# Kernel tuning notes

Measured on AMD Instinct MI355X. Metric: run time of the kernel, lower is better.

The kernel has to match this reference:

```python
import jax, jax.numpy as jnp
import numpy as np

COST_W = {'cls': 1.0, 'center': 0.0, 'obj_ness': 0.0, 'giou': 2.0}
IOU_THRES = 0.25
MAX_DYN = 10
EPS = 1e-6
N_PRED, N_GT, N_CLS = 65536, 128, 256


def _to_bbox(centers, sizes):
    # center/size -> (x1,y1,z1,x2,y2,z2)
    return jnp.concatenate([centers - sizes / 2.0, centers + sizes / 2.0], axis=-1)


def _giou_3d(b1, b2):
    # b1 [N,6], b2 [M,6] -> giou [N,M] (axis_aligned_bbox_overlaps_3d, mode='giou')
    vol1 = jnp.prod(b1[:, 3:] - b1[:, :3], axis=-1)  # [N]
    vol2 = jnp.prod(b2[:, 3:] - b2[:, :3], axis=-1)  # [M]
    lt = jnp.maximum(b1[:, None, :3], b2[None, :, :3])  # [N,M,3]
    rb = jnp.minimum(b1[:, None, 3:], b2[None, :, 3:])
    overlap = jnp.prod(jnp.clip(rb - lt, 0.0), axis=-1)  # [N,M]
    union = jnp.maximum(vol1[:, None] + vol2[None, :] - overlap, EPS)
    iou = overlap / union
    elt = jnp.minimum(b1[:, None, :3], b2[None, :, :3])
    erb = jnp.maximum(b1[:, None, 3:], b2[None, :, 3:])
    enclose = jnp.maximum(jnp.prod(jnp.clip(erb - elt, 0.0), axis=-1), EPS)
    return iou - (enclose - union) / enclose


def _lsa(cost):
    # Jonker-Volgenant shortest-augmenting-path LAP (same optimum as
    # scipy.optimize.linear_sum_assignment). cost [n, m], n <= m.
    # Returns col4row[n]: column matched to each row.
    n, m = cost.shape
    u = np.zeros(n, np.float64)
    v = np.zeros(m, np.float64)
    col4row = np.full(n, -1, np.int64)
    row4col = np.full(m, -1, np.int64)
    cost = cost.astype(np.float64)
    for cur in range(n):
        shortest = np.full(m, np.inf)
        path = np.full(m, -1, np.int64)
        SC = np.zeros(m, bool)
        SR = []
        i, min_val, sink = cur, 0.0, -1
        while sink == -1:
            SR.append(i)
            r = min_val + cost[i] - u[i] - v
            upd = (~SC) & (r < shortest)
            shortest = np.where(upd, r, shortest)
            path = np.where(upd, i, path)
            masked = np.where(SC, np.inf, shortest)
            j = int(masked.argmin())
            min_val = masked[j]
            SC[j] = True
            if row4col[j] == -1:
                sink = j
            else:
                i = int(row4col[j])
        u[cur] += min_val
        for i2 in SR:
            if i2 != cur:
                u[i2] += min_val - shortest[col4row[i2]]
        v[SC] -= min_val - shortest[SC]
        j = sink
        while True:
            i2 = int(path[j])
            row4col[j] = i2
            col4row[i2], j = j, col4row[i2]
            if i2 == cur:
                break
    return col4row


def _dynamic_assign(giou, used0, order):
    # Sequential greedy IoU-threshold assignment over gts (ascending max-iou).
    NEG = jnp.float32(-1e9)
    n_pred = giou.shape[0]

    def step(used, gt_idx):
        col = giou[:, gt_idx]
        vals = jnp.where((col > IOU_THRES) & (~used), col, NEG)
        topv, topi = jax.lax.top_k(vals, MAX_DYN)
        valid = topv > NEG
        used = used | jnp.zeros((n_pred,), bool).at[topi].set(valid)
        return used, (jnp.where(valid, topi, -1), jnp.where(valid, gt_idx, -1))

    _, (dp, dg) = jax.lax.scan(step, used0, order)
    return dp.reshape(-1), dg.reshape(-1)  # padded with -1 where invalid


def setup_inputs() -> dict:
    key = jax.random.key(0)
    k = jax.random.split(key, 7)
    return {
        'all_centers': jax.random.normal(k[0], (N_PRED, 3), jnp.float32),
        'all_sizes': jax.random.uniform(k[1], (N_PRED, 3), jnp.float32),
        'all_cls': jax.random.normal(k[2], (N_PRED, N_CLS), jnp.float32),
        'all_objness': jax.random.normal(k[3], (N_PRED,), jnp.float32),
        'gt_centers': jax.random.normal(k[4], (N_GT, 3), jnp.float32),
        'gt_sizes': jax.random.uniform(k[5], (N_GT, 3), jnp.float32),
        'gt_labels': jax.random.randint(k[6], (N_GT,), 0, N_CLS, jnp.int64),
    }


def reference(all_centers, all_sizes, all_cls, all_objness, gt_centers, gt_sizes, gt_labels):
    pred_bbox = _to_bbox(all_centers, all_sizes)
    gt_bbox = _to_bbox(gt_centers, gt_sizes)
    giou = _giou_3d(pred_bbox, gt_bbox)  # [N, M]
    cost_class = -jax.nn.sigmoid(all_cls)[:, gt_labels]  # [N, M]
    cost_center = jnp.sum(jnp.abs(all_centers[:, None, :] - gt_centers[None, :, :]), axis=-1)  # cdist p=1
    cost_obj = -jax.nn.sigmoid(all_objness)[:, None]  # [N, 1]
    total_cost = (COST_W['cls'] * cost_class + COST_W['center'] * cost_center
                  + COST_W['obj_ness'] * cost_obj + COST_W['giou'] * (-giou))
    # Hungarian on transposed cost (M <= N): same optimal pairing as scipy on [N, M].
    col4row = _lsa(np.asarray(jax.device_get(total_cost)).T)
    pred_indices = jnp.asarray(col4row, jnp.int64)       # matched pred per gt
    gt_indices = jnp.arange(gt_labels.shape[0], dtype=jnp.int64)
    used0 = jnp.zeros((giou.shape[0],), bool).at[pred_indices].set(True)
    order = jnp.argsort(jnp.max(giou, axis=0))
    dp, dg = _dynamic_assign(giou, used0, order)
    combined_preds = jnp.concatenate([pred_indices, dp.astype(jnp.int64)])
    combined_gts = jnp.concatenate([gt_indices, dg.astype(jnp.int64)])
    return combined_preds, combined_gts
```

## Files before the change

kernel.cpp:

```cpp
#include <hip/hip_runtime.h>
#include <hip/hip_bf16.h>
#include <math.h>

#define NPRED 65536
#define NGT   128
#define NCLS  256
#define CAP   12288
#define VCAP  160
#define VSLOT 129
#define NLIST 129
#define LSTRIDE 132
#define KEEP  2048
#define KMIN  1418
#define GSPLIT 4
#define GPB   (NGT / GSPLIT)
#define SENT_I 0x7FFFFFFF


__device__ __forceinline__ unsigned f2u(float f) {
    unsigned u = __float_as_uint(f);
    return (u & 0x80000000u) ? ~u : (u | 0x80000000u);
}
__device__ __forceinline__ float u2f(unsigned x) {
    unsigned u = (x & 0x80000000u) ? (x ^ 0x80000000u) : ~x;
    return __uint_as_float(u);
}
__device__ __forceinline__ unsigned long long d2u(double d) {
    unsigned long long u = (unsigned long long)__double_as_longlong(d);
    return (u & 0x8000000000000000ull) ? ~u : (u | 0x8000000000000000ull);
}
__device__ __forceinline__ double u2d(unsigned long long x) {
    unsigned long long u = (x & 0x8000000000000000ull) ? (x ^ 0x8000000000000000ull) : ~x;
    return __longlong_as_double((long long)u);
}

__device__ __forceinline__ float giou3d(
    float pl0, float pl1, float pl2, float ph0, float ph1, float ph2, float pvol,
    float gl0, float gl1, float gl2, float gh0, float gh1, float gh2, float gvol)
{
#pragma clang fp contract(off)
    float c0 = fmaxf(fminf(ph0, gh0) - fmaxf(pl0, gl0), 0.0f);
    float c1 = fmaxf(fminf(ph1, gh1) - fmaxf(pl1, gl1), 0.0f);
    float c2 = fmaxf(fminf(ph2, gh2) - fmaxf(pl2, gl2), 0.0f);
    float overlap = (c0 * c1) * c2;
    float uni = fmaxf((pvol + gvol) - overlap, 1e-6f);
    float iou = overlap / uni;
    float e0 = fmaxf(fmaxf(ph0, gh0) - fminf(pl0, gl0), 0.0f);
    float e1 = fmaxf(fmaxf(ph1, gh1) - fminf(pl1, gl1), 0.0f);
    float e2 = fmaxf(fmaxf(ph2, gh2) - fminf(pl2, gl2), 0.0f);
    float enc = fmaxf((e0 * e1) * e2, 1e-6f);
    return iou - (enc - uni) / enc;
}


__global__ __launch_bounds__(256) void k_gather(
    const float* __restrict__ cls, const int* __restrict__ lab,
    float* __restrict__ costT,
    int* __restrict__ ccnt, unsigned* __restrict__ cmax, int* __restrict__ failFlag)
{
#pragma clang fp contract(off)
    __shared__ float tile[64][NCLS + 1];
    __shared__ int labl[NGT];
    int tid = threadIdx.x;
    int p0 = blockIdx.x * 64;
    if (blockIdx.x == 0) {
        if (tid < NGT) { ccnt[tid] = 0; cmax[tid] = 0u; }
        if (tid == 0) *failFlag = 0;
    }
    if (tid < NGT) labl[tid] = lab[tid];
    for (int it = 0; it < 16; ++it) {
        int row = it * 4 + (tid >> 6);
        int col = (tid & 63) * 4;
        const float4 v = *(const float4*)&cls[(size_t)(p0 + row) * NCLS + col];
        tile[row][col + 0] = v.x; tile[row][col + 1] = v.y;
        tile[row][col + 2] = v.z; tile[row][col + 3] = v.w;
    }
    __syncthreads();
    int lane = tid & 63;
    for (int rep = 0; rep < 32; ++rep) {
        int g = rep * 4 + (tid >> 6);
        float val = tile[lane][labl[g]];
        double s = 1.0 / (1.0 + exp(-(double)val));
        costT[(size_t)g * NPRED + p0 + lane] = -(float)s;
    }
}

__global__ __launch_bounds__(256) void k_cost(
    const float* __restrict__ pc, const float* __restrict__ ps,
    const float* __restrict__ gc, const float* __restrict__ gs,
    float* __restrict__ costT, int* __restrict__ ccnt, unsigned* __restrict__ cmax,
    int2* __restrict__ cpair)
{
#pragma clang fp contract(off)
    __shared__ float gb[GPB][6];
    __shared__ float gvol[GPB];
    __shared__ unsigned smax[GPB];
    __shared__ int cntl[GPB], basel[GPB], curl[GPB];
    int tid = threadIdx.x;
    int lane = tid & 63;
    int g0 = (blockIdx.x & (GSPLIT - 1)) * GPB;
    int p  = (blockIdx.x >> 2) * 256 + tid;

    if (tid < GPB) {
        int g = g0 + tid;
        float c0 = gc[g * 3 + 0], c1 = gc[g * 3 + 1], c2 = gc[g * 3 + 2];
        float s0 = gs[g * 3 + 0], s1 = gs[g * 3 + 1], s2 = gs[g * 3 + 2];
        float l0 = c0 - s0 / 2.0f, l1 = c1 - s1 / 2.0f, l2 = c2 - s2 / 2.0f;
        float h0 = c0 + s0 / 2.0f, h1 = c1 + s1 / 2.0f, h2 = c2 + s2 / 2.0f;
        gb[tid][0] = l0; gb[tid][1] = l1; gb[tid][2] = l2;
        gb[tid][3] = h0; gb[tid][4] = h1; gb[tid][5] = h2;
        gvol[tid] = ((h0 - l0) * (h1 - l1)) * (h2 - l2);
        smax[tid] = 0u; cntl[tid] = 0; curl[tid] = 0;
    }
    __syncthreads();

    float c0 = pc[p * 3 + 0], c1 = pc[p * 3 + 1], c2 = pc[p * 3 + 2];
    float s0 = ps[p * 3 + 0], s1 = ps[p * 3 + 1], s2 = ps[p * 3 + 2];
    float pl0 = c0 - s0 / 2.0f, pl1 = c1 - s1 / 2.0f, pl2 = c2 - s2 / 2.0f;
    float ph0 = c0 + s0 / 2.0f, ph1 = c1 + s1 / 2.0f, ph2 = c2 + s2 / 2.0f;
    float pvol = ((ph0 - pl0) * (ph1 - pl1)) * (ph2 - pl2);

    for (int gg = 0; gg < GPB; ++gg) {
        float gio = giou3d(pl0, pl1, pl2, ph0, ph1, ph2, pvol,
                           gb[gg][0], gb[gg][1], gb[gg][2], gb[gg][3], gb[gg][4], gb[gg][5],
                           gvol[gg]);
        float m = gio;
        for (int off = 32; off; off >>= 1) m = fmaxf(m, __shfl_xor(m, off, 64));
        unsigned long long mask = __ballot(gio > 0.25f);
        if (lane == 0) {
            atomicMax(&smax[gg], f2u(m));
            atomicAdd(&cntl[gg], __popcll(mask));
        }
        size_t ij = (size_t)(g0 + gg) * NPRED + p;
        float ns = costT[ij];
        costT[ij] = ns + (2.0f * (-gio));
    }
    __syncthreads();
    if (tid < GPB) {
        atomicMax(&cmax[g0 + tid], smax[tid]);
        basel[tid] = atomicAdd(&ccnt[g0 + tid], cntl[tid]);
    }
    __syncthreads();

    for (int gg = 0; gg < GPB; ++gg) {
        float gio = giou3d(pl0, pl1, pl2, ph0, ph1, ph2, pvol,
                           gb[gg][0], gb[gg][1], gb[gg][2], gb[gg][3], gb[gg][4], gb[gg][5],
                           gvol[gg]);
        bool cand = (gio > 0.25f);
        unsigned long long mask = __ballot(cand);
        int cnt = __popcll(mask);
        int wo = 0;
        if (lane == 0 && cnt) wo = atomicAdd(&curl[gg], cnt);
        wo = __shfl(wo, 0, 64);
        if (cand) {
            int slot = basel[gg] + wo + __popcll(mask & ((1ull << lane) - 1ull));
            if (slot < CAP)
                cpair[(size_t)(g0 + gg) * CAP + slot] = make_int2(p, __float_as_int(gio));
        }
    }
}

__global__ __launch_bounds__(128) void k_sort(const unsigned* __restrict__ cmax,
                                              int* __restrict__ order) {
    __shared__ unsigned m[NGT];
    int t = threadIdx.x;
    m[t] = cmax[t];
    __syncthreads();
    unsigned mt = m[t];
    int r = 0;
    for (int k = 0; k < NGT; ++k) {
        unsigned mk = m[k];
        if (mk < mt || (mk == mt && k < t)) r++;
    }
    order[r] = t;
}

__global__ __launch_bounds__(256) void k_toprow(
    const float* __restrict__ costT, int2* __restrict__ rowlist)
{
    __shared__ unsigned long long keys[2048];
    __shared__ int hist[256];
    __shared__ unsigned long long sh_prefix;
    __shared__ int sh_rank, sh_cnt, sh_ok;
    int tid = threadIdx.x;
    int row = blockIdx.x;
    const float* crow = costT + (size_t)row * NPRED;

    unsigned long long lv[8];
#pragma unroll
    for (int q = 0; q < 8; ++q) lv[q] = ~0ull;
    const float4* crow4 = (const float4*)crow;
    for (int it = tid; it < NPRED / 4; it += 256) {
        float4 v4 = crow4[it];
        int j = it * 4;
        float vv[4] = {v4.x, v4.y, v4.z, v4.w};
#pragma unroll
        for (int e = 0; e < 4; ++e) {
            unsigned long long key =
                ((unsigned long long)f2u(vv[e]) << 32) | (unsigned)(j + e);
            if (key < lv[7]) {
                unsigned long long c = key;
#pragma unroll
                for (int q = 0; q < 8; ++q) {
                    unsigned long long mx = (c > lv[q]) ? c : lv[q];
                    unsigned long long mn = (c > lv[q]) ? lv[q] : c;
                    lv[q] = mn; c = mx;
                }
            }
        }
    }
#pragma unroll
    for (int q = 0; q < 8; ++q) keys[tid * 8 + q] = lv[q];
    if (tid == 0) sh_ok = 1;
    __syncthreads();

    for (int k = 2; k <= 2048; k <<= 1) {
        for (int j2 = k >> 1; j2 > 0; j2 >>= 1) {
            for (int i = tid; i < 2048; i += 256) {
                int ixj = i ^ j2;
                if (ixj > i) {
                    unsigned long long a = keys[i], b2 = keys[ixj];
                    bool up = ((i & k) == 0);
                    if ((up && a > b2) || (!up && a < b2)) { keys[i] = b2; keys[ixj] = a; }
                }
            }
            __syncthreads();
        }
    }

    unsigned long long thr = keys[NLIST - 1];
    if (lv[7] < thr) sh_ok = 0;
    __syncthreads();

    if (sh_ok) {
        if (tid < NLIST) {
            unsigned long long key = keys[tid];
            rowlist[row * LSTRIDE + tid] =
                make_int2(__float_as_int(u2f((unsigned)(key >> 32))),
                          (int)(unsigned)(key & 0xFFFFFFFFull));
        }
        return;
    }

    if (tid == 0) { sh_prefix = 0ull; sh_rank = NLIST - 1; sh_cnt = 0; }
    __syncthreads();
    for (int d = 7; d >= 0; --d) {
        hist[tid] = 0;
        __syncthreads();
        unsigned long long pref = sh_prefix;
        int sh = (d + 1) * 8;
        for (int j = tid; j < NPRED; j += 256) {
            unsigned long long key = ((unsigned long long)f2u(crow[j]) << 32) | (unsigned)j;
            bool match = (sh >= 64) || ((key >> sh) == (pref >> sh));
            if (match) atomicAdd(&hist[(int)((key >> (d * 8)) & 255ull)], 1);
        }
        __syncthreads();
        if (tid == 0) {
            int rank = sh_rank, cum = 0, b = 0;
            for (; b < 256; ++b) { if (cum + hist[b] > rank) break; cum += hist[b]; }
            sh_prefix = pref | ((unsigned long long)b << (d * 8));
            sh_rank = rank - cum;
        }
        __syncthreads();
    }
    unsigned long long thr2 = sh_prefix;
    for (int j = tid; j < NPRED; j += 256) {
        unsigned long long key = ((unsigned long long)f2u(crow[j]) << 32) | (unsigned)j;
        if (key <= thr2) { int s = atomicAdd(&sh_cnt, 1); keys[s] = key; }
    }
    __syncthreads();
    if (tid >= sh_cnt) keys[tid] = ~0ull;
    __syncthreads();
    for (int k = 2; k <= 256; k <<= 1) {
        for (int j2 = k >> 1; j2 > 0; j2 >>= 1) {
            int i = tid, ixj = i ^ j2;
            if (ixj > i) {
                unsigned long long a = keys[i], b2 = keys[ixj];
                bool up = ((i & k) == 0);
                if ((up && a > b2) || (!up && a < b2)) { keys[i] = b2; keys[ixj] = a; }
            }
            __syncthreads();
        }
    }
    if (tid < NLIST) {
        unsigned long long key = keys[tid];
        rowlist[row * LSTRIDE + tid] =
            make_int2(__float_as_int(u2f((unsigned)(key >> 32))),
                      (int)(unsigned)(key & 0xFFFFFFFFull));
    }
}

__global__ __launch_bounds__(64) void k_lsa_sparse(
    const float* __restrict__ costT, const int2* __restrict__ rowlist,
    int* __restrict__ failFlag,
    unsigned* __restrict__ usedbits, int* __restrict__ out)
{
#pragma clang fp contract(off)
    __shared__ float  costV[NGT][VSLOT];
    __shared__ double u_l[NGT];
    __shared__ int    c4r[NGT];
    __shared__ int    slot4row[NGT];
    __shared__ int    headpos[NGT];
    __shared__ int    colidV[VCAP];
    __shared__ double vV[VCAP], shortV[VCAP];
    __shared__ int    pathV[VCAP], r4cV[VCAP];
    __shared__ unsigned char SCV[VCAP];
    __shared__ int    SRr[VCAP];
    __shared__ double headv[VCAP];
    __shared__ int    headj[VCAP];
    __shared__ unsigned vbits[2048];
    __shared__ int S_bi, S_sink, S_nSR, S_nV, S_fail, S_pendrow, S_pendpos;
    __shared__ double S_mv, S_pendmv;

    int lane = threadIdx.x;
    for (int w = lane; w < 2048; w += 64) vbits[w] = 0u;
    for (int r = lane; r < NGT; r += 64) {
        u_l[r] = 0.0; c4r[r] = -1; slot4row[r] = -1; headpos[r] = 0;
    }
    if (lane == 0) { S_nV = 0; S_fail = 0; }
    __syncthreads();

    for (int cur = 0; cur < NGT; ++cur) {
        int nV0 = S_nV;
        for (int k = lane; k < nV0; k += 64) { shortV[k] = INFINITY; pathV[k] = -1; SCV[k] = 0; }
        if (lane == 0) {
            S_bi = cur; S_sink = -1; S_mv = 0.0;
            SRr[0] = cur; S_nSR = 1;
            S_pendrow = cur; S_pendpos = 0; S_pendmv = 0.0;
        }
        __syncthreads();

        while (true) {
            int prow = S_pendrow;
            if (prow >= 0) {
                int pos = headpos[prow];
                float hval = 0.0f; int hcol = SENT_I;
                while (pos < NLIST) {
                    int i = pos + lane;
                    int2 e = (i < NLIST) ? rowlist[prow * LSTRIDE + i] : make_int2(0, SENT_I);
                    int c = e.y;
                    bool fresh = (i < NLIST) && !((vbits[c >> 5] >> (c & 31)) & 1u);
                    unsigned long long m = __ballot(fresh);
                    if (m) {
                        int fl = __ffsll(m) - 1;
                        hcol = __shfl(c, fl, 64);
                        hval = __shfl(__int_as_float(e.x), fl, 64);
                        pos += fl;
                        break;
                    }
                    pos += 64;
                }
                if (lane == 0) {
                    headpos[prow] = pos;
                    int pp = S_pendpos;
                    headj[pp] = hcol;
                    headv[pp] = (hcol == SENT_I) ? (double)INFINITY
                                                 : ((S_pendmv + (double)hval) - u_l[prow]);
                    S_pendrow = -1;
                }
                __syncthreads();
            }

            int bi = S_bi; double mv = S_mv; int nV = S_nV; int s = S_nSR;
            double ui = u_l[bi];
            double bv = (double)INFINITY; int bj = SENT_I, bp = SENT_I, baux = -1, bisv = 0;
            for (int k = lane; k < nV; k += 64) {
                if (!SCV[k]) {
                    double c = (double)costV[bi][k];
                    double r = ((mv + c) - ui) - vV[k];
                    if (r < shortV[k]) { shortV[k] = r; pathV[k] = bi; }
                    double sval = shortV[k]; int scol = colidV[k];
                    if (sval < bv || (sval == bv && scol < bj)) {
                        bv = sval; bj = scol; bp = SENT_I; baux = k; bisv = 1;
                    }
                }
            }
            for (int p = lane; p < s; p += 64) {
                double hv = headv[p]; int hj = headj[p];
                if (hv < bv || (hv == bv && (hj < bj || (hj == bj && p < bp)))) {
                    bv = hv; bj = hj; bp = p; baux = p; bisv = 0;
                }
            }
            {
                unsigned long long vkey = d2u(bv);
                unsigned long long mkey = vkey;
#pragma unroll
                for (int off = 1; off < 64; off <<= 1) {
                    unsigned long long o = __shfl_xor(mkey, off, 64);
                    if (o < mkey) mkey = o;
                }
                unsigned long long tiedm = __ballot(vkey == mkey);
                int W;
                if (__popcll(tiedm) > 1) {
                    unsigned long long tkey = (vkey == mkey)
                        ? (((unsigned long long)(unsigned)bj << 32) | (unsigned)bp)
                        : ~0ull;
                    unsigned long long mt = tkey;
#pragma unroll
                    for (int off = 1; off < 64; off <<= 1) {
                        unsigned long long o = __shfl_xor(mt, off, 64);
                        if (o < mt) mt = o;
                    }
                    W = __ffsll(__ballot(tkey == mt)) - 1;
                } else {
                    W = __ffsll(tiedm) - 1;
                }
                bv = u2d(mkey);
                bj = __shfl(bj, W, 64);
                baux = __shfl(baux, W, 64);
                bisv = __shfl(bisv, W, 64);
            }
            if (lane == 0) {
                S_mv = bv;
                if (bisv) {
                    SCV[baux] = 1;
                    int nr = r4cV[baux];
                    SRr[s] = nr;
                    headv[s] = (double)INFINITY; headj[s] = SENT_I;
                    S_pendrow = nr; S_pendpos = s; S_pendmv = bv;
                    S_nSR = s + 1; S_bi = nr;
                } else {
                    int k2 = S_nV;
                    if (k2 >= VCAP) S_fail = 1;
                    else {
                        colidV[k2] = bj; vV[k2] = 0.0; shortV[k2] = bv;
                        pathV[k2] = SRr[baux]; SCV[k2] = 1; r4cV[k2] = -1;
                        vbits[bj >> 5] |= (1u << (bj & 31));
                        S_nV = k2 + 1;
                        S_sink = bj;
                    }
                }
            }
            __syncthreads();
            if (S_sink >= 0 || S_fail) break;
        }
        if (S_fail) break;

        int snew = S_nV - 1;
        int cnew = S_sink;
        float pfa = costT[(size_t)lane * NPRED + cnew];
        float pfb = costT[(size_t)(lane + 64) * NPRED + cnew];

        double mvf = S_mv;
        int nVn = S_nV;
        for (int k = lane; k < nVn; k += 64)
            if (SCV[k]) vV[k] -= (mvf - shortV[k]);
        if (lane == 0) {
            u_l[cur] += mvf;
            int s = S_nSR;
            for (int q = 1; q < s; ++q) {
                int i2 = SRr[q];
                u_l[i2] += mvf - shortV[slot4row[i2]];
            }
            int jslot = S_nV - 1;
            while (true) {
                int i2 = pathV[jslot];
                r4cV[jslot] = i2;
                int oldslot = (c4r[i2] >= 0) ? slot4row[i2] : -1;
                c4r[i2] = colidV[jslot];
                slot4row[i2] = jslot;
                if (i2 == cur) break;
                jslot = oldslot;
            }
        }
        costV[lane][snew]      = pfa;
        costV[lane + 64][snew] = pfb;
        __syncthreads();
    }

    if (lane == 0 && S_fail) *failFlag = 1;
    __syncthreads();
    if (!S_fail) {
        for (int w = lane; w < 2048; w += 64) usedbits[w] = 0u;
        __syncthreads();
        for (int r = lane; r < NGT; r += 64) {
            int p = c4r[r];
            atomicOr(&usedbits[p >> 5], 1u << (p & 31));
            out[r] = p;
            out[1408 + r] = r;
        }
    }
}

__global__ __launch_bounds__(1024) void k_lsa_dense(
    const float* __restrict__ costT, const int* __restrict__ failFlag,
    double* __restrict__ v, double* __restrict__ shortest,
    int* __restrict__ path, int* __restrict__ row4col,
    unsigned char* __restrict__ SC, unsigned* __restrict__ usedbits,
    int* __restrict__ out)
{
#pragma clang fp contract(off)
    if (*failFlag == 0) return;
    __shared__ double u_l[NGT];
    __shared__ int    c4r[NGT];
    __shared__ int    SR[NGT + 1];
    __shared__ int    bi, bsink, nSR;
    __shared__ double bmin;
    __shared__ double wval[16];
    __shared__ int    widx[16];
    int tid = threadIdx.x;

    for (int j = tid; j < NPRED; j += 1024) { v[j] = 0.0; row4col[j] = -1; }
    if (tid < NGT) { u_l[tid] = 0.0; c4r[tid] = -1; }
    __syncthreads();

    for (int cur = 0; cur < NGT; ++cur) {
        for (int j = tid; j < NPRED; j += 1024) {
            shortest[j] = (double)INFINITY; path[j] = -1; SC[j] = 0;
        }
        if (tid == 0) { bi = cur; bsink = -1; bmin = 0.0; SR[0] = cur; nSR = 1; }
        __syncthreads();

        while (true) {
            int irow = bi;
            double mv = bmin;
            double ui = u_l[irow];
            const float* crow = costT + (size_t)irow * NPRED;
            double bestv = (double)INFINITY;
            int    bestj = SENT_I;
            for (int j = tid; j < NPRED; j += 1024) {
                if (!SC[j]) {
                    double s = shortest[j];
                    double r = ((mv + (double)crow[j]) - ui) - v[j];
                    if (r < s) { s = r; shortest[j] = r; path[j] = irow; }
                    if (s < bestv || (s == bestv && j < bestj)) { bestv = s; bestj = j; }
                }
            }
            for (int off = 32; off; off >>= 1) {
                double ov = __shfl_down(bestv, off, 64);
                int    oj = __shfl_down(bestj, off, 64);
                if (ov < bestv || (ov == bestv && oj < bestj)) { bestv = ov; bestj = oj; }
            }
            if ((tid & 63) == 0) { wval[tid >> 6] = bestv; widx[tid >> 6] = bestj; }
            __syncthreads();
            if (tid == 0) {
                double bv = wval[0]; int bj = widx[0];
                for (int w = 1; w < 16; ++w) {
                    double ov = wval[w]; int oj = widx[w];
                    if (ov < bv || (ov == bv && oj < bj)) { bv = ov; bj = oj; }
                }
                bmin = bv;
                SC[bj] = 1;
                int r = row4col[bj];
                if (r < 0) { bsink = bj; }
                else       { SR[nSR++] = r; bi = r; }
            }
            __syncthreads();
            if (bsink >= 0) break;
        }

        double mv = bmin;
        for (int j = tid; j < NPRED; j += 1024)
            if (SC[j]) v[j] -= (mv - shortest[j]);
        if (tid == 0) {
            u_l[cur] += mv;
            for (int k = 1; k < nSR; ++k) {
                int i2 = SR[k];
                u_l[i2] += mv - shortest[c4r[i2]];
            }
            int j = bsink;
            while (true) {
                int i2 = path[j];
                row4col[j] = i2;
                int nj = c4r[i2];
                c4r[i2] = j;
                j = nj;
                if (i2 == cur) break;
            }
        }
        __syncthreads();
    }

    for (int w = tid; w < 2048; w += 1024) usedbits[w] = 0u;
    __syncthreads();
    for (int j = tid; j < NPRED; j += 1024)
        if (row4col[j] >= 0) atomicOr(&usedbits[j >> 5], 1u << (j & 31));
    if (tid < NGT) {
        out[tid]        = c4r[tid];
        out[1408 + tid] = tid;
    }
}

__global__ __launch_bounds__(256) void k_prep(
    const int2* __restrict__ cpair, const int* __restrict__ ccnt,
    unsigned long long* __restrict__ scand, int* __restrict__ kcount,
    int* __restrict__ fullflag)
{
    __shared__ int hist[256];
    __shared__ unsigned long long keys[KEEP];
    __shared__ unsigned sh_pref, sh_thresh;
    __shared__ int sh_done, sh_fail, sh_cnt;
    int tid = threadIdx.x;
    int g = blockIdx.x;
    int nc = ccnt[g]; if (nc > CAP) nc = CAP;
    const int2* src = cpair + (size_t)g * CAP;

    unsigned thresh = 0;
    if (nc > KEEP - 1) {
        if (tid == 0) { sh_pref = 0; sh_done = 0; sh_fail = 0; }
        __syncthreads();
        int above = 0;
        for (int byt = 3; byt >= 0; --byt) {
            hist[tid] = 0;
            __syncthreads();
            unsigned pref = sh_pref;
            for (int c = tid; c < nc; c += 256) {
                unsigned u = f2u(__int_as_float(src[c].y));
                if (byt == 3 || (u >> ((byt + 1) * 8)) == (pref >> ((byt + 1) * 8)))
                    atomicAdd(&hist[(u >> (byt * 8)) & 255], 1);
            }
            __syncthreads();
            if (tid == 0) {
                int cum = 0, B = 0, kept = 0, abnew = above;
                for (int b = 255; b >= 0; --b) {
                    if (above + cum + hist[b] >= KMIN) {
                        B = b; kept = above + cum + hist[b]; abnew = above + cum; break;
                    }
                    cum += hist[b];
                }
                if (kept <= KEEP - 1) { sh_thresh = sh_pref | ((unsigned)B << (byt * 8)); sh_done = 1; }
                else {
                    above = abnew;
                    sh_pref = sh_pref | ((unsigned)B << (byt * 8));
                    if (byt == 0) sh_fail = 1;
                }
            }
            __syncthreads();
            if (sh_done || sh_fail) break;
        }
        if (sh_fail) {
            if (tid == 0) { fullflag[g] = 1; kcount[g] = 0; }
            return;
        }
        thresh = sh_thresh;
    }
    if (tid == 0) sh_cnt = 0;
    __syncthreads();
    for (int c = tid; c < nc; c += 256) {
        unsigned u = f2u(__int_as_float(src[c].y));
        if (u >= thresh) {
            int slot = atomicAdd(&sh_cnt, 1);
            keys[slot] = ((unsigned long long)(~u) << 32) | (unsigned)src[c].x;
        }
    }
    __syncthreads();
    int kept = sh_cnt;
    for (int i = tid; i < KEEP; i += 256) if (i >= kept) keys[i] = ~0ull;
    __syncthreads();
    for (int k = 2; k <= KEEP; k <<= 1) {
        for (int j = k >> 1; j > 0; j >>= 1) {
            for (int i = tid; i < KEEP; i += 256) {
                int ixj = i ^ j;
                if (ixj > i) {
                    unsigned long long a = keys[i], b = keys[ixj];
                    bool up = ((i & k) == 0);
                    if ((up && a > b) || (!up && a < b)) { keys[i] = b; keys[ixj] = a; }
                }
            }
            __syncthreads();
        }
    }
    for (int i = tid; i < KEEP; i += 256) scand[(size_t)g * KEEP + i] = keys[i];
    if (tid == 0) { kcount[g] = kept; fullflag[g] = 0; }
}

__global__ __launch_bounds__(64) void k_dyn2(
    const int* __restrict__ order, const int* __restrict__ kcount,
    const unsigned long long* __restrict__ scand, const int* __restrict__ fullflag,
    const int* __restrict__ ccnt, const int2* __restrict__ cpair,
    const unsigned* __restrict__ usedbits_g, const int* __restrict__ failFlag,
    int* __restrict__ out)
{
    __shared__ unsigned bits[2048];
    int lane = threadIdx.x;
    for (int w = lane; w < 2048; w += 64) bits[w] = usedbits_g[w];
    __syncthreads();
    bool globalFull = (*failFlag != 0);

    for (int k = 0; k < NGT; ++k) {
        int gt = order[k];
        int got = 0;
        if (!globalFull && fullflag[gt] == 0) {
            int kept = kcount[gt];
            int base = 0;
            while (got < 10 && base < kept) {
                int i = base + lane;
                unsigned long long key = (i < kept) ? scand[(size_t)gt * KEEP + i] : ~0ull;
                int p = (int)(unsigned)(key & 0xFFFFFFFFull);
                bool ok = (key != ~0ull) && !((bits[p >> 5] >> (p & 31)) & 1u);
                unsigned long long mask = __ballot(ok);
                int need = 10 - got;
                int pre = __popcll(mask & ((1ull << lane) - 1ull));
                if (ok && pre < need) {
                    out[128 + k * 10 + got + pre] = p;
                    out[1408 + 128 + k * 10 + got + pre] = gt;
                    atomicOr(&bits[p >> 5], 1u << (p & 31));
                }
                int tot = __popcll(mask);
                got += (tot < need) ? tot : need;
                base += 64;
                __syncthreads();
            }
        } else {
            int nc = ccnt[gt]; if (nc > CAP) nc = CAP;
            float lv[10]; int li[10];
#pragma unroll
            for (int q = 0; q < 10; ++q) { lv[q] = -1e30f; li[q] = SENT_I; }
            for (int c = lane; c < nc; c += 64) {
                int2 pr = cpair[(size_t)gt * CAP + c];
                int p = pr.x;
                if ((bits[p >> 5] >> (p & 31)) & 1u) continue;
                float cv = __int_as_float(pr.y); int ci = p;
#pragma unroll
                for (int q = 0; q < 10; ++q) {
                    bool b = (cv > lv[q]) || (cv == lv[q] && ci < li[q]);
                    float tv = b ? lv[q] : cv; int ti = b ? li[q] : ci;
                    if (b) { lv[q] = cv; li[q] = ci; }
                    cv = tv; ci = ti;
                }
            }
#pragma unroll
            for (int q = 0; q < 10; ++q) {
                float mo = lv[0]; int mj = li[0];
#pragma unroll
                for (int off = 1; off < 64; off <<= 1) {
                    float ov = __shfl_xor(mo, off, 64);
                    int oj = __shfl_xor(mj, off, 64);
                    if (ov > mo || (ov == mo && oj < mj)) { mo = ov; mj = oj; }
                }
                bool valid = (mj != SENT_I);
                if (valid && li[0] == mj) {
#pragma unroll
                    for (int t = 0; t < 9; ++t) { lv[t] = lv[t + 1]; li[t] = li[t + 1]; }
                    lv[9] = -1e30f; li[9] = SENT_I;
                }
                if (lane == q) {
                    out[128 + k * 10 + q] = valid ? mj : -1;
                    out[1408 + 128 + k * 10 + q] = valid ? gt : -1;
                    if (valid) atomicOr(&bits[mj >> 5], 1u << (mj & 31));
                }
            }
            got = 10;
            __syncthreads();
        }
        for (int q = got + lane; q < 10; q += 64) {
            out[128 + k * 10 + q] = -1;
            out[1408 + 128 + k * 10 + q] = -1;
        }
        __syncthreads();
    }
}


extern "C" void kernel_launch(void* const* d_in, const int* in_sizes, int n_in,
                              void* d_out, int out_size, void* d_ws, size_t ws_size,
                              hipStream_t stream) {
    const float* pc  = (const float*)d_in[0];
    const float* ps  = (const float*)d_in[1];
    const float* cls = (const float*)d_in[2];
    const float* gc  = (const float*)d_in[4];
    const float* gs  = (const float*)d_in[5];
    const int*   lab = (const int*)d_in[6];

    char* ws = (char*)d_ws;
    float*         costT    = (float*)(ws + 0);
    unsigned long long* scand = (unsigned long long*)(ws + 0);
    int2*          rowlist  = (int2*)(ws + 33554432);
    double*        v        = (double*)(ws + 33554432);
    double*        shortest = (double*)(ws + 34078720);
    int*           path     = (int*)(ws + 34603008);
    int*           row4col  = (int*)(ws + 34865152);
    unsigned char* SC       = (unsigned char*)(ws + 35127296);
    int*           kcount   = (int*)(ws + 35192832);
    int*           fullflag = (int*)(ws + 35193344);
    int*           ccnt     = (int*)(ws + 35193856);
    unsigned*      cmax     = (unsigned*)(ws + 35194368);
    int*           order    = (int*)(ws + 35194880);
    int*           failFlag = (int*)(ws + 35195392);
    unsigned*      usedbits = (unsigned*)(ws + 35195904);
    int2*          cpair    = (int2*)(ws + 35204096);

    int* out = (int*)d_out;

    hipLaunchKernelGGL(k_gather, dim3(NPRED / 64), dim3(256), 0, stream,
                       cls, lab, costT, ccnt, cmax, failFlag);
    hipLaunchKernelGGL(k_cost, dim3((NPRED / 256) * GSPLIT), dim3(256), 0, stream,
                       pc, ps, gc, gs, costT, ccnt, cmax, cpair);
    hipLaunchKernelGGL(k_sort, dim3(1), dim3(128), 0, stream, cmax, order);
    hipLaunchKernelGGL(k_toprow, dim3(NGT), dim3(256), 0, stream, costT, rowlist);
    hipLaunchKernelGGL(k_lsa_sparse, dim3(1), dim3(64), 0, stream,
                       costT, rowlist, failFlag, usedbits, out);
    hipLaunchKernelGGL(k_lsa_dense, dim3(1), dim3(1024), 0, stream,
                       costT, failFlag, v, shortest, path, row4col, SC, usedbits, out);
    hipLaunchKernelGGL(k_prep, dim3(NGT), dim3(256), 0, stream,
                       cpair, ccnt, scand, kcount, fullflag);
    hipLaunchKernelGGL(k_dyn2, dim3(1), dim3(64), 0, stream,
                       order, kcount, scand, fullflag, ccnt, cpair, usedbits, failFlag, out);
}
```

Before: 760.9 us.

## Cache GIoU values in registers and fold pending-head scan into LAP argmin

In the candidate kernel, GIoU values from the first pass are kept in a per-thread register array, so the second pass no longer recomputes giou3d. The loop is fully unrolled. In the single-wave Hungarian loop, the separate pending-row head-scan phase and its __syncthreads are removed. The head lookup is now prefetched and merged into the same iteration's argmin, which shortens the serial dependency chain per augmenting step. The risks are higher register pressure from the 32-entry array and a subtler ordering of the pending head against the other candidates. The merged path also reads headpos[prow] even when prow may be negative.

```diff
diff --git a/kernel.cpp b/kernel.cpp
--- a/kernel.cpp
+++ b/kernel.cpp
@@ -120,10 +120,14 @@
     float ph0 = c0 + s0 / 2.0f, ph1 = c1 + s1 / 2.0f, ph2 = c2 + s2 / 2.0f;
     float pvol = ((ph0 - pl0) * (ph1 - pl1)) * (ph2 - pl2);
 
+    float gior[GPB];
+
+#pragma unroll
     for (int gg = 0; gg < GPB; ++gg) {
         float gio = giou3d(pl0, pl1, pl2, ph0, ph1, ph2, pvol,
                            gb[gg][0], gb[gg][1], gb[gg][2], gb[gg][3], gb[gg][4], gb[gg][5],
                            gvol[gg]);
+        gior[gg] = gio;
         float m = gio;
         for (int off = 32; off; off >>= 1) m = fmaxf(m, __shfl_xor(m, off, 64));
         unsigned long long mask = __ballot(gio > 0.25f);
@@ -142,10 +146,9 @@
     }
     __syncthreads();
 
+#pragma unroll
     for (int gg = 0; gg < GPB; ++gg) {
-        float gio = giou3d(pl0, pl1, pl2, ph0, ph1, ph2, pvol,
-                           gb[gg][0], gb[gg][1], gb[gg][2], gb[gg][3], gb[gg][4], gb[gg][5],
-                           gvol[gg]);
+        float gio = gior[gg];
         bool cand = (gio > 0.25f);
         unsigned long long mask = __ballot(cand);
         int cnt = __popcll(mask);
@@ -332,36 +335,15 @@
 
         while (true) {
             int prow = S_pendrow;
-            if (prow >= 0) {
-                int pos = headpos[prow];
-                float hval = 0.0f; int hcol = SENT_I;
-                while (pos < NLIST) {
-                    int i = pos + lane;
-                    int2 e = (i < NLIST) ? rowlist[prow * LSTRIDE + i] : make_int2(0, SENT_I);
-                    int c = e.y;
-                    bool fresh = (i < NLIST) && !((vbits[c >> 5] >> (c & 31)) & 1u);
-                    unsigned long long m = __ballot(fresh);
-                    if (m) {
-                        int fl = __ffsll(m) - 1;
-                        hcol = __shfl(c, fl, 64);
-                        hval = __shfl(__int_as_float(e.x), fl, 64);
-                        pos += fl;
-                        break;
-                    }
-                    pos += 64;
-                }
-                if (lane == 0) {
-                    headpos[prow] = pos;
-                    int pp = S_pendpos;
-                    headj[pp] = hcol;
-                    headv[pp] = (hcol == SENT_I) ? (double)INFINITY
-                                                 : ((S_pendmv + (double)hval) - u_l[prow]);
-                    S_pendrow = -1;
-                }
-                __syncthreads();
-            }
-
+            int pp   = S_pendpos;
+            double pmv = S_pendmv;
             int bi = S_bi; double mv = S_mv; int nV = S_nV; int s = S_nSR;
+
+            int pos = headpos[prow];
+            int i0 = pos + lane;
+            int2 e0 = (i0 < NLIST) ? rowlist[prow * LSTRIDE + i0]
+                                   : make_int2(0, SENT_I);
+
             double ui = u_l[bi];
             double bv = (double)INFINITY; int bj = SENT_I, bp = SENT_I, baux = -1, bisv = 0;
             for (int k = lane; k < nV; k += 64) {
@@ -376,11 +358,49 @@
                 }
             }
             for (int p = lane; p < s; p += 64) {
+                if (p == pp) continue;
                 double hv = headv[p]; int hj = headj[p];
                 if (hv < bv || (hv == bv && (hj < bj || (hj == bj && p < bp)))) {
                     bv = hv; bj = hj; bp = p; baux = p; bisv = 0;
                 }
             }
+
+            int hcol = SENT_I; float hval = 0.0f;
+            {
+                int c0 = e0.y;
+                bool fresh = (i0 < NLIST) && !((vbits[c0 >> 5] >> (c0 & 31)) & 1u);
+                unsigned long long m0 = __ballot(fresh);
+                if (m0) {
+                    int fl = __ffsll(m0) - 1;
+                    hcol = __shfl(c0, fl, 64);
+                    hval = __shfl(__int_as_float(e0.x), fl, 64);
+                    pos += fl;
+                } else {
+                    pos += 64;
+                    while (pos < NLIST) {
+                        int i = pos + lane;
+                        int2 e = (i < NLIST) ? rowlist[prow * LSTRIDE + i] : make_int2(0, SENT_I);
+                        int c = e.y;
+                        bool fr = (i < NLIST) && !((vbits[c >> 5] >> (c & 31)) & 1u);
+                        unsigned long long m = __ballot(fr);
+                        if (m) {
+                            int fl = __ffsll(m) - 1;
+                            hcol = __shfl(c, fl, 64);
+                            hval = __shfl(__int_as_float(e.x), fl, 64);
+                            pos += fl;
+                            break;
+                        }
+                        pos += 64;
+                    }
+                }
+            }
+            double pend_headv = (hcol == SENT_I) ? (double)INFINITY
+                                : ((pmv + (double)hval) - u_l[prow]);
+            if (pend_headv < bv ||
+                (pend_headv == bv && (hcol < bj || (hcol == bj && pp < bp)))) {
+                bv = pend_headv; bj = hcol; bp = pp; baux = pp; bisv = 0;
+            }
+
             {
                 unsigned long long vkey = d2u(bv);
                 unsigned long long mkey = vkey;
@@ -410,7 +430,10 @@
                 baux = __shfl(baux, W, 64);
                 bisv = __shfl(bisv, W, 64);
             }
+
             if (lane == 0) {
+                headpos[prow] = pos;
+                headv[pp] = pend_headv; headj[pp] = hcol;
                 S_mv = bv;
                 if (bisv) {
                     SCV[baux] = 1;
```

Result: faster. 736.1 us (-3.3%).
